# Kernel tuning notes

Measured on AMD Instinct MI355X. Metric: run time of the kernel, lower is better.

Reference implementation:

```python
import jax, jax.numpy as jnp
import numpy as np

QMAX = 127.0

def fake_quant(x):
    # per-tensor symmetric int8 fake quantize-dequantize (QAT)
    s = jnp.maximum(jnp.max(jnp.abs(x)) / QMAX, 1e-8)
    q = jnp.clip(jnp.round(x / s), -QMAX, QMAX) * s
    return x + jax.lax.stop_gradient(q - x)  # STE

def qlinear(x, w, b):
    # x already fake-quantized by caller (input_quantizer); weights fake-quantized here
    return jnp.einsum('btc,oc->bto', x, fake_quant(w)) + b

def layer_norm(x, g, b, eps=1e-5):
    m = jnp.mean(x, axis=-1, keepdims=True)
    v = jnp.var(x, axis=-1, keepdims=True)
    return (x - m) * jax.lax.rsqrt(v + eps) * g + b

def setup_inputs() -> dict:
    key = jax.random.key(0)
    ks = jax.random.split(key, 8)
    B, T, C, I = 8, 512, 1024, 4096
    sd = 0.02
    return {
        'hidden_states': jax.random.normal(ks[0], (B, T, C), jnp.float32),
        'attention_mask': jnp.ones((B, T), jnp.float32),
        'ln1_g': jnp.ones((C,), jnp.float32), 'ln1_b': jnp.zeros((C,), jnp.float32),
        'ln2_g': jnp.ones((C,), jnp.float32), 'ln2_b': jnp.zeros((C,), jnp.float32),
        'w_qkv': sd * jax.random.normal(ks[1], (3 * C, C), jnp.float32),
        'b_qkv': jnp.zeros((3 * C,), jnp.float32),
        'w_out': sd * jax.random.normal(ks[2], (C, C), jnp.float32),
        'b_out': jnp.zeros((C,), jnp.float32),
        'w1': sd * jax.random.normal(ks[3], (I, C), jnp.float32),
        'b1': jnp.zeros((I,), jnp.float32),
        'w2': sd * jax.random.normal(ks[4], (C, I), jnp.float32),
        'b2': jnp.zeros((C,), jnp.float32),
    }

def reference(hidden_states, attention_mask, ln1_g, ln1_b, ln2_g, ln2_b,
              w_qkv, b_qkv, w_out, b_out, w1, b1, w2, b2):
    B, T, C = hidden_states.shape
    H = 16
    Dh = C // H
    scale = Dh ** -0.5

    # --- attention branch (pre-norm) ---
    x = layer_norm(hidden_states, ln1_g, ln1_b)
    qkv = qlinear(fake_quant(x), w_qkv, b_qkv)            # [B,T,3C]
    qkv = qkv.reshape(B, T, 3, H, Dh).transpose(2, 0, 3, 1, 4)
    q, k, v = qkv[0], qkv[1], qkv[2]                       # [B,H,T,Dh]
    scores = jnp.einsum('bhqd,bhkd->bhqk', q, k) * scale
    ext = (1.0 - attention_mask)[:, None, None, :] * -10000.0
    scores = scores + ext
    attn = jax.nn.softmax(scores, axis=-1)
    out = jnp.einsum('bhqk,bhkd->bhqd', attn, v)
    out = out.transpose(0, 2, 1, 3).reshape(B, T, C)
    attn_out = qlinear(fake_quant(out), w_out, b_out)
    h = hidden_states + attn_out

    # --- MLP branch (pre-norm) ---
    x = layer_norm(h, ln2_g, ln2_b)
    x = qlinear(fake_quant(x), w1, b1)
    x = jax.nn.gelu(x, approximate=False)
    x = qlinear(fake_quant(x), w2, b2)
    return h + x
```

## Files before the change

kernel.cpp:

```cpp
#include <hip/hip_runtime.h>

typedef __attribute__((ext_vector_type(8))) short bf16x8;
typedef __attribute__((ext_vector_type(4))) float f32x4;
typedef __attribute__((ext_vector_type(4))) int i32x4;
typedef unsigned short u16;
typedef unsigned int u32;

#define B_ 8
#define T_ 512
#define C_ 1024
#define I_ 4096
#define H_ 16
#define Dh_ 64
#define BT (B_*T_)
#define NH (B_*H_)

__device__ __forceinline__ float bf2f(u16 u) {
  return __uint_as_float(((u32)u) << 16);
}
__device__ __forceinline__ u16 f2bf(float f) {
  u32 u = __float_as_uint(f);
  u32 r = u + 0x7FFFu + ((u >> 16) & 1u);
  return (u16)(r >> 16);
}
__device__ __forceinline__ float wredMax(float v) {
#pragma unroll
  for (int o = 32; o; o >>= 1) v = fmaxf(v, __shfl_xor(v, o));
  return v;
}
__device__ __forceinline__ float wredSum(float v) {
#pragma unroll
  for (int o = 32; o; o >>= 1) v += __shfl_xor(v, o);
  return v;
}
__device__ __forceinline__ void slotAtomicMax(u32* arr, int bid, float bm) {
  u32 b = __float_as_uint(bm);
  volatile u32* p = arr + ((bid & 63) << 4);
  if (b > *p) atomicMax((u32*)p, b);
}
__device__ __forceinline__ float slotMax(const u32* __restrict__ arr) {
  float m = 0.f;
#pragma unroll
  for (int i = 0; i < 64; ++i) m = fmaxf(m, __uint_as_float(arr[i << 4]));
  return m;
}
__device__ __forceinline__ void gload16(const void* g, void* l) {
  __builtin_amdgcn_global_load_lds((const __attribute__((address_space(1))) void*)g,
                                   (__attribute__((address_space(3))) void*)l, 16, 0, 0);
}
__device__ __forceinline__ int qi(float v, float inv) {
  return (int)fminf(fmaxf(rintf(v * inv), -127.f), 127.f);
}

__global__ void k_init(u32* s) {
  int i = blockIdx.x * 256 + threadIdx.x;
  if (i < 8192) s[i] = 0u;
}

__global__ __launch_bounds__(256) void k_absmax4(
    const float* __restrict__ p0, int n0,
    const float* __restrict__ p1, int n1,
    const float* __restrict__ p2, int n2,
    const float* __restrict__ p3, int n3,
    u32* __restrict__ sc) {
  int stride = gridDim.x * blockDim.x;
  int gid = blockIdx.x * blockDim.x + threadIdx.x;
  float m0 = 0.f, m1 = 0.f, m2 = 0.f, m3 = 0.f;
  for (int i = gid; i < n0; i += stride) {
    float4 v = ((const float4*)p0)[i];
    m0 = fmaxf(m0, fmaxf(fmaxf(fabsf(v.x), fabsf(v.y)), fmaxf(fabsf(v.z), fabsf(v.w))));
  }
  for (int i = gid; i < n1; i += stride) {
    float4 v = ((const float4*)p1)[i];
    m1 = fmaxf(m1, fmaxf(fmaxf(fabsf(v.x), fabsf(v.y)), fmaxf(fabsf(v.z), fabsf(v.w))));
  }
  for (int i = gid; i < n2; i += stride) {
    float4 v = ((const float4*)p2)[i];
    m2 = fmaxf(m2, fmaxf(fmaxf(fabsf(v.x), fabsf(v.y)), fmaxf(fabsf(v.z), fabsf(v.w))));
  }
  for (int i = gid; i < n3; i += stride) {
    float4 v = ((const float4*)p3)[i];
    m3 = fmaxf(m3, fmaxf(fmaxf(fabsf(v.x), fabsf(v.y)), fmaxf(fabsf(v.z), fabsf(v.w))));
  }
  m0 = wredMax(m0); m1 = wredMax(m1); m2 = wredMax(m2); m3 = wredMax(m3);
  __shared__ float red[4][4];
  int wid = threadIdx.x >> 6, lane = threadIdx.x & 63;
  if (lane == 0) { red[wid][0] = m0; red[wid][1] = m1; red[wid][2] = m2; red[wid][3] = m3; }
  __syncthreads();
  if (threadIdx.x < 4) {
    int j = threadIdx.x;
    float bm = fmaxf(fmaxf(red[0][j], red[1][j]), fmaxf(red[2][j], red[3][j]));
    slotAtomicMax(sc + j * 1024, blockIdx.x, bm);
  }
}

__global__ __launch_bounds__(256) void k_quant4(
    const float* __restrict__ p0, signed char* __restrict__ q0, int n0,
    const float* __restrict__ p1, signed char* __restrict__ q1, int n1,
    const float* __restrict__ p2, signed char* __restrict__ q2, int n2,
    const float* __restrict__ p3, signed char* __restrict__ q3, int n3,
    const u32* __restrict__ sc) {
  int stride = gridDim.x * blockDim.x;
  int gid = blockIdx.x * blockDim.x + threadIdx.x;
#define QLOOP(p, q, n, slot)                                                        \
  {                                                                                 \
    float s = fmaxf(slotMax(sc + slot * 1024) * (1.0f / 127.0f), 1e-8f);            \
    float inv = 1.0f / s;                                                           \
    for (int i = gid; i < n; i += stride) {                                         \
      float4 v = ((const float4*)p)[i];                                             \
      u32 pk = (u32)(qi(v.x, inv) & 255) | ((u32)(qi(v.y, inv) & 255) << 8) |       \
               ((u32)(qi(v.z, inv) & 255) << 16) | ((u32)(qi(v.w, inv) & 255) << 24); \
      ((u32*)q)[i] = pk;                                                            \
    }                                                                               \
  }
  QLOOP(p0, q0, n0, 0)
  QLOOP(p1, q1, n1, 1)
  QLOOP(p2, q2, n2, 2)
  QLOOP(p3, q3, n3, 3)
#undef QLOOP
}

__global__ __launch_bounds__(256) void k_quant_b8(const u16* __restrict__ x, signed char* __restrict__ q,
                                                  int n8, const u32* __restrict__ arr) {
  float s = fmaxf(slotMax(arr) * (1.0f / 127.0f), 1e-8f);
  float inv = 1.0f / s;
  int stride = gridDim.x * blockDim.x;
  for (int i = blockIdx.x * blockDim.x + threadIdx.x; i < n8; i += stride) {
    uint4 d = ((const uint4*)x)[i];
    u16* e = (u16*)&d;
    uint2 o;
    o.x = (u32)(qi(bf2f(e[0]), inv) & 255) | ((u32)(qi(bf2f(e[1]), inv) & 255) << 8) |
          ((u32)(qi(bf2f(e[2]), inv) & 255) << 16) | ((u32)(qi(bf2f(e[3]), inv) & 255) << 24);
    o.y = (u32)(qi(bf2f(e[4]), inv) & 255) | ((u32)(qi(bf2f(e[5]), inv) & 255) << 8) |
          ((u32)(qi(bf2f(e[6]), inv) & 255) << 16) | ((u32)(qi(bf2f(e[7]), inv) & 255) << 24);
    ((uint2*)q)[i] = o;
  }
}

__global__ __launch_bounds__(256) void k_ln(const float* __restrict__ x, const float* __restrict__ g,
                                            const float* __restrict__ b, u16* __restrict__ y,
                                            u32* __restrict__ arr) {
  int row = blockIdx.x;
  int t = threadIdx.x;
  float4 v = ((const float4*)(x + (long)row * C_))[t];
  float s1 = v.x + v.y + v.z + v.w;
  float s2 = v.x * v.x + v.y * v.y + v.z * v.z + v.w * v.w;
  s1 = wredSum(s1);
  s2 = wredSum(s2);
  __shared__ float red[8];
  int wid = t >> 6, lane = t & 63;
  if (lane == 0) { red[wid] = s1; red[4 + wid] = s2; }
  __syncthreads();
  s1 = red[0] + red[1] + red[2] + red[3];
  s2 = red[4] + red[5] + red[6] + red[7];
  float mean = s1 * (1.0f / C_);
  float var = s2 * (1.0f / C_) - mean * mean;
  float inv = rsqrtf(var + 1e-5f);
  float4 gv = ((const float4*)g)[t];
  float4 bv = ((const float4*)b)[t];
  float4 o;
  o.x = (v.x - mean) * inv * gv.x + bv.x;
  o.y = (v.y - mean) * inv * gv.y + bv.y;
  o.z = (v.z - mean) * inv * gv.z + bv.z;
  o.w = (v.w - mean) * inv * gv.w + bv.w;
  ushort4 ob;
  ob.x = f2bf(o.x); ob.y = f2bf(o.y); ob.z = f2bf(o.z); ob.w = f2bf(o.w);
  ((ushort4*)(y + (long)row * C_))[t] = ob;
  float m = fmaxf(fmaxf(fabsf(o.x), fabsf(o.y)), fmaxf(fabsf(o.z), fabsf(o.w)));
  m = wredMax(m);
  __syncthreads();
  if (lane == 0) red[wid] = m;
  __syncthreads();
  if (t == 0) {
    float bm = fmaxf(fmaxf(red[0], red[1]), fmaxf(red[2], red[3]));
    slotAtomicMax(arr, row, bm);
  }
}

__global__ __launch_bounds__(256, 1) void k_attn(
    const u16* __restrict__ qkv, const float* __restrict__ mask,
    u16* __restrict__ O, u32* __restrict__ amax) {
  __shared__ u16 Ke[512 * 64];
  __shared__ u16 Vt[64 * 512];
  __shared__ u16 Pl[4 * 64 * 40];
  __shared__ float extl[512];
  __shared__ float redm[4];
  const int tid = threadIdx.x;
  const int w = tid >> 6, l = tid & 63;
  const int head = blockIdx.x;
  const int chunk = blockIdx.y;
  const int b = head >> 4, h = head & 15;
  const long rowbase = (long)(b * 512) * (3 * C_);

  {
    const u16* Kg = qkv + rowbase + C_ + h * 64;
    int lr8 = l >> 3;
    int ls = (l & 7) ^ lr8;
    const long koff = (long)lr8 * (3 * C_) + ls * 8;
#pragma unroll
    for (int i = 0; i < 16; ++i) {
      int r0 = w * 128 + i * 8;
      gload16(Kg + (long)r0 * (3 * C_) + koff, &Ke[r0 * 64]);
    }
  }
  {
    const u16* Vg = qkv + rowbase + 2 * C_ + h * 64;
    int kvl = tid & 31;
    int d0 = (tid >> 5) * 8;
#pragma unroll 4
    for (int i = 0; i < 16; ++i) {
      int kv = i * 32 + kvl;
      uint4 t4 = *(const uint4*)(Vg + (long)kv * (3 * C_) + d0);
      u16* tv = (u16*)&t4;
      int slot = kv >> 3, within = kv & 7;
#pragma unroll
      for (int j = 0; j < 8; ++j) {
        int d = d0 + j;
        Vt[d * 512 + ((slot ^ (d & 7)) << 3) + within] = tv[j];
      }
    }
  }
  {
    const float* mb = mask + b * 512;
    extl[tid] = (1.0f - mb[tid]) * -10000.0f;
    extl[tid + 256] = (1.0f - mb[tid + 256]) * -10000.0f;
  }
  const int qbase = chunk * 256 + w * 64;
  bf16x8 qf[4][2];
  {
    const u16* Qg = qkv + rowbase + h * 64;
#pragma unroll
    for (int qt = 0; qt < 4; ++qt)
#pragma unroll
      for (int dc = 0; dc < 2; ++dc)
        qf[qt][dc] = *(const bf16x8*)(Qg + (long)(qbase + qt * 16 + (l & 15)) * (3 * C_) + dc * 32 + (l >> 4) * 8);
  }
  __syncthreads();

  f32x4 oacc[4][4];
  float mrun[4], lrun[4];
#pragma unroll
  for (int qt = 0; qt < 4; ++qt) { mrun[qt] = -3.0e38f; lrun[qt] = 0.f; }
#pragma unroll
  for (int dt = 0; dt < 4; ++dt)
#pragma unroll
    for (int qt = 0; qt < 4; ++qt) oacc[dt][qt] = (f32x4){0.f, 0.f, 0.f, 0.f};

  u16* Pw = &Pl[w * 64 * 40];

  for (int ks = 0; ks < 16; ++ks) {
    bf16x8 kf[2][2];
#pragma unroll
    for (int kvt = 0; kvt < 2; ++kvt) {
      int kv = ks * 32 + kvt * 16 + (l & 15);
#pragma unroll
      for (int dc = 0; dc < 2; ++dc) {
        int phys = (dc * 4 + (l >> 4)) ^ (kv & 7);
        kf[kvt][dc] = *(const bf16x8*)&Ke[kv * 64 + phys * 8];
      }
    }
    f32x4 sacc[2][4];
#pragma unroll
    for (int kvt = 0; kvt < 2; ++kvt)
#pragma unroll
      for (int qt = 0; qt < 4; ++qt) {
        f32x4 a = (f32x4){0.f, 0.f, 0.f, 0.f};
        a = __builtin_amdgcn_mfma_f32_16x16x32_bf16(kf[kvt][0], qf[qt][0], a, 0, 0, 0);
        a = __builtin_amdgcn_mfma_f32_16x16x32_bf16(kf[kvt][1], qf[qt][1], a, 0, 0, 0);
        sacc[kvt][qt] = a;
      }
#pragma unroll
    for (int kvt = 0; kvt < 2; ++kvt) {
      f32x4 ev = *(const f32x4*)&extl[ks * 32 + kvt * 16 + (l >> 4) * 4];
#pragma unroll
      for (int qt = 0; qt < 4; ++qt)
#pragma unroll
        for (int r = 0; r < 4; ++r)
          sacc[kvt][qt][r] = fmaf(sacc[kvt][qt][r], 0.125f, ev[r]);
    }
#pragma unroll
    for (int qt = 0; qt < 4; ++qt) {
      float pm = sacc[0][qt][0];
#pragma unroll
      for (int r = 1; r < 4; ++r) pm = fmaxf(pm, sacc[0][qt][r]);
#pragma unroll
      for (int r = 0; r < 4; ++r) pm = fmaxf(pm, sacc[1][qt][r]);
      pm = fmaxf(pm, __shfl_xor(pm, 16));
      pm = fmaxf(pm, __shfl_xor(pm, 32));
      float mnew = fmaxf(mrun[qt], pm);
      float f = __expf(mrun[qt] - mnew);
      mrun[qt] = mnew;
      float lsum = 0.f;
#pragma unroll
      for (int kvt = 0; kvt < 2; ++kvt)
#pragma unroll
        for (int r = 0; r < 4; ++r) {
          float p = __expf(sacc[kvt][qt][r] - mnew);
          sacc[kvt][qt][r] = p;
          lsum += p;
        }
      lsum += __shfl_xor(lsum, 16);
      lsum += __shfl_xor(lsum, 32);
      lrun[qt] = lrun[qt] * f + lsum;
#pragma unroll
      for (int dt = 0; dt < 4; ++dt)
#pragma unroll
        for (int r = 0; r < 4; ++r) oacc[dt][qt][r] *= f;
#pragma unroll
      for (int kvt = 0; kvt < 2; ++kvt) {
        u32 p01 = (u32)f2bf(sacc[kvt][qt][0]) | ((u32)f2bf(sacc[kvt][qt][1]) << 16);
        u32 p23 = (u32)f2bf(sacc[kvt][qt][2]) | ((u32)f2bf(sacc[kvt][qt][3]) << 16);
        u16* pr = Pw + (qt * 16 + (l & 15)) * 40 + kvt * 16 + (l >> 4) * 4;
        *(u32*)pr = p01;
        *(u32*)(pr + 2) = p23;
      }
    }
    bf16x8 vf[4], pf[4];
#pragma unroll
    for (int dt = 0; dt < 4; ++dt) {
      int d = dt * 16 + (l & 15);
      int phys = (ks * 4 + (l >> 4)) ^ (d & 7);
      vf[dt] = *(const bf16x8*)&Vt[d * 512 + phys * 8];
    }
#pragma unroll
    for (int qt = 0; qt < 4; ++qt)
      pf[qt] = *(const bf16x8*)(Pw + (qt * 16 + (l & 15)) * 40 + (l >> 4) * 8);
#pragma unroll
    for (int dt = 0; dt < 4; ++dt)
#pragma unroll
      for (int qt = 0; qt < 4; ++qt)
        oacc[dt][qt] = __builtin_amdgcn_mfma_f32_16x16x32_bf16(vf[dt], pf[qt], oacc[dt][qt], 0, 0, 0);
  }

  float lmax = 0.f;
  u16* Ob = O + (long)(b * 512 + qbase) * C_ + h * 64;
#pragma unroll
  for (int qt = 0; qt < 4; ++qt) {
    float inv = 1.0f / lrun[qt];
    long qoff = (long)(qt * 16 + (l & 15)) * C_;
#pragma unroll
    for (int dt = 0; dt < 4; ++dt) {
      int d = dt * 16 + (l >> 4) * 4;
      float v0 = oacc[dt][qt][0] * inv;
      float v1 = oacc[dt][qt][1] * inv;
      float v2 = oacc[dt][qt][2] * inv;
      float v3 = oacc[dt][qt][3] * inv;
      lmax = fmaxf(fmaxf(lmax, fmaxf(fabsf(v0), fabsf(v1))), fmaxf(fabsf(v2), fabsf(v3)));
      u32 a01 = (u32)f2bf(v0) | ((u32)f2bf(v1) << 16);
      u32 a23 = (u32)f2bf(v2) | ((u32)f2bf(v3) << 16);
      *(u32*)(Ob + qoff + d) = a01;
      *(u32*)(Ob + qoff + d + 2) = a23;
    }
  }
  lmax = wredMax(lmax);
  if (l == 0) redm[w] = lmax;
  __syncthreads();
  if (tid == 0)
    slotAtomicMax(amax, blockIdx.x * 2 + blockIdx.y,
                  fmaxf(fmaxf(redm[0], redm[1]), fmaxf(redm[2], redm[3])));
}

template <int BM, int BN, int EPI, bool SWZ>
__global__ __launch_bounds__(256) void k_gemmq(
    const signed char* __restrict__ A, int lda,
    const signed char* __restrict__ Bm, int ldb,
    const float* __restrict__ bias,
    void* __restrict__ Cp, int ldc,
    int M, int N, int K,
    const float* __restrict__ resid,
    u32* __restrict__ amaxOut,
    const u32* __restrict__ amaxA, const u32* __restrict__ amaxB) {
  constexpr int BK = 128;
  constexpr int MF = (BM / 2) / 16;
  constexpr int NF = (BN / 2) / 16;
  __shared__ __align__(16) signed char As[2][BM * BK];
  __shared__ __align__(16) signed char Bs[2][BN * BK];
  const int tid = threadIdx.x;
  const int wid = tid >> 6, lane = tid & 63;
  const int wr = wid >> 1, wc = wid & 1;

  float sa = fmaxf(slotMax(amaxA) * (1.0f / 127.0f), 1e-8f);
  float sb = fmaxf(slotMax(amaxB) * (1.0f / 127.0f), 1e-8f);
  const float sAB = sa * sb;

  int bx = blockIdx.x, by = blockIdx.y;
  if (SWZ) {
    int gx = gridDim.x;
    int nwg = gx * gridDim.y;
    int bid = by * gx + bx;
    int cpx = nwg >> 3;
    int swz = (bid & 7) * cpx + (bid >> 3);
    bx = swz % gx;
    by = swz / gx;
  }

  const signed char* Ab = A + (long)by * BM * lda;
  const signed char* Bb = Bm + (long)bx * BN * ldb;

  i32x4 acc[MF][NF];
#pragma unroll
  for (int m = 0; m < MF; m++)
#pragma unroll
    for (int n = 0; n < NF; n++) acc[m][n] = (i32x4){0, 0, 0, 0};

  const int lr = lane & 15;
  const int l8 = lane >> 3;
  const int s8 = (lane & 7) ^ l8;
  const long aoff = (long)l8 * lda + s8 * 16;
  const long boff = (long)l8 * ldb + s8 * 16;

  auto stageAB = [&](int buf, int k0) {
#pragma unroll
    for (int i = 0; i < BM / 32; ++i) {
      int R0 = wid * (BM / 4) + i * 8;
      gload16(Ab + (long)R0 * lda + k0 + aoff, &As[buf][R0 * BK]);
    }
#pragma unroll
    for (int i = 0; i < BN / 32; ++i) {
      int R0 = wid * (BN / 4) + i * 8;
      gload16(Bb + (long)R0 * ldb + k0 + boff, &Bs[buf][R0 * BK]);
    }
  };

  auto waitCounted = [&]() {
    if constexpr ((BM / 32 + BN / 32) == 8) {
      asm volatile("s_waitcnt vmcnt(8)" ::: "memory");
    } else {
      asm volatile("s_waitcnt vmcnt(6)" ::: "memory");
    }
  };

  auto computeK = [&](int buf) {
#pragma unroll
    for (int kk = 0; kk < 2; ++kk) {
      const int sl = (kk << 2) + (lane >> 4);
      const int sf = (sl ^ (lr & 7)) << 4;
      i32x4 af[MF], bfr[NF];
#pragma unroll
      for (int m = 0; m < MF; m++)
        af[m] = *(const i32x4*)&As[buf][(wr * (BM / 2) + m * 16 + lr) * BK + sf];
#pragma unroll
      for (int n = 0; n < NF; n++)
        bfr[n] = *(const i32x4*)&Bs[buf][(wc * (BN / 2) + n * 16 + lr) * BK + sf];
      __builtin_amdgcn_s_setprio(1);
#pragma unroll
      for (int m = 0; m < MF; m++)
#pragma unroll
        for (int n = 0; n < NF; n++)
          acc[m][n] = __builtin_amdgcn_mfma_i32_16x16x64_i8(af[m], bfr[n], acc[m][n], 0, 0, 0);
      __builtin_amdgcn_s_setprio(0);
    }
  };

  const int nt = K / BK;
  stageAB(0, 0);
  int cur = 0;
  for (int t = 0; t < nt; ++t) {
    if (t + 1 < nt) {
      stageAB(cur ^ 1, (t + 1) * BK);
      waitCounted();
    } else {
      asm volatile("s_waitcnt vmcnt(0)" ::: "memory");
    }
    __builtin_amdgcn_s_barrier();
    computeK(cur);
    if (t + 1 < nt)
      __builtin_amdgcn_s_barrier();
    cur ^= 1;
  }

  const int rowBase = by * BM + wr * (BM / 2);
  const int colBase = bx * BN + wc * (BN / 2);
  float lmax = 0.f;
#pragma unroll
  for (int m = 0; m < MF; m++) {
    int row0 = rowBase + m * 16 + (lane >> 4) * 4;
#pragma unroll
    for (int n = 0; n < NF; n++) {
      int col = colBase + n * 16 + lr;
      float bs = bias[col];
#pragma unroll
      for (int j = 0; j < 4; j++) {
        int row = row0 + j;
        long idx = (long)row * ldc + col;
        float v = (float)acc[m][n][j] * sAB;
        if (EPI == 0) {
          ((u16*)Cp)[idx] = f2bf(v + bs);
        } else if (EPI == 1) {
          ((float*)Cp)[idx] = v + bs + resid[idx];
        } else if (EPI == 2) {
          v += bs;
          float x2 = v * v;
          float e = __expf(v * fmaf(-0.0713548755f, x2, -1.5957691216f));
          v = v * __builtin_amdgcn_rcpf(1.0f + e);
          lmax = fmaxf(fmaxf(lmax, v), 0.0f - v);
          ((u16*)Cp)[idx] = f2bf(v);
        } else if (EPI == 3) {
          ((float*)Cp)[idx] = v + bs + resid[idx];
        }
      }
    }
  }
  if (EPI == 2) {
    __shared__ float redm[4];
    float wm = wredMax(lmax);
    if (lane == 0) redm[wid] = wm;
    __syncthreads();
    if (tid == 0) {
      float bm = fmaxf(fmaxf(redm[0], redm[1]), fmaxf(redm[2], redm[3]));
      slotAtomicMax(amaxOut, blockIdx.y * gridDim.x + blockIdx.x, bm);
    }
  }
}

extern "C" void kernel_launch(void* const* d_in, const int* in_sizes, int n_in,
                              void* d_out, int out_size, void* d_ws, size_t ws_size,
                              hipStream_t stream) {
  const float* hidden = (const float*)d_in[0];
  const float* mask = (const float*)d_in[1];
  const float* ln1g = (const float*)d_in[2];
  const float* ln1b = (const float*)d_in[3];
  const float* ln2g = (const float*)d_in[4];
  const float* ln2b = (const float*)d_in[5];
  const float* w_qkv = (const float*)d_in[6];
  const float* b_qkv = (const float*)d_in[7];
  const float* w_out = (const float*)d_in[8];
  const float* b_out = (const float*)d_in[9];
  const float* w1 = (const float*)d_in[10];
  const float* b1 = (const float*)d_in[11];
  const float* w2 = (const float*)d_in[12];
  const float* b2 = (const float*)d_in[13];

  char* ws = (char*)d_ws;
  u32* sc = (u32*)ws;
  const long MB = 1024 * 1024;
  signed char* wq_qkv = (signed char*)(ws + 1 * MB);
  signed char* wq_out = (signed char*)(ws + 4 * MB);
  signed char* wq_w1  = (signed char*)(ws + 6 * MB);
  signed char* wq_w2  = (signed char*)(ws + 10 * MB);
  signed char* xq     = (signed char*)(ws + 14 * MB);
  u16* x1             = (u16*)(ws + 18 * MB);
  signed char* Oq     = (signed char*)(ws + 26 * MB);
  u16* O              = (u16*)(ws + 30 * MB);
  u16* qkv            = (u16*)(ws + 38 * MB);
  float* hbuf         = (float*)(ws + 62 * MB);
  u16* y1             = (u16*)(ws + 78 * MB);
  signed char* y1q    = (signed char*)(ws + 110 * MB);

  k_init<<<32, 256, 0, stream>>>(sc);

  k_absmax4<<<512, 256, 0, stream>>>(
      w_qkv, 3 * C_ * C_ / 4, w_out, C_ * C_ / 4, w1, I_ * C_ / 4, w2, C_ * I_ / 4, sc);
  k_quant4<<<512, 256, 0, stream>>>(
      w_qkv, wq_qkv, 3 * C_ * C_ / 4, w_out, wq_out, C_ * C_ / 4,
      w1, wq_w1, I_ * C_ / 4, w2, wq_w2, C_ * I_ / 4, sc);

  k_ln<<<BT, 256, 0, stream>>>(hidden, ln1g, ln1b, x1, sc + 4 * 1024);
  k_quant_b8<<<512, 256, 0, stream>>>(x1, xq, BT * C_ / 8, sc + 4 * 1024);

  k_gemmq<128, 128, 0, true><<<dim3(24, 32), 256, 0, stream>>>(
      xq, C_, wq_qkv, C_, b_qkv, qkv, 3 * C_,
      BT, 3 * C_, C_, nullptr, nullptr, sc + 4 * 1024, sc + 0 * 1024);

  k_attn<<<dim3(NH, 2), 256, 0, stream>>>(qkv, mask, O, sc + 5 * 1024);
  k_quant_b8<<<512, 256, 0, stream>>>(O, Oq, BT * C_ / 8, sc + 5 * 1024);

  k_gemmq<64, 128, 1, true><<<dim3(8, 64), 256, 0, stream>>>(
      Oq, C_, wq_out, C_, b_out, hbuf, C_,
      BT, C_, C_, hidden, nullptr, sc + 5 * 1024, sc + 1 * 1024);

  k_ln<<<BT, 256, 0, stream>>>(hbuf, ln2g, ln2b, x1, sc + 6 * 1024);
  k_quant_b8<<<512, 256, 0, stream>>>(x1, xq, BT * C_ / 8, sc + 6 * 1024);

  k_gemmq<128, 128, 2, true><<<dim3(32, 32), 256, 0, stream>>>(
      xq, C_, wq_w1, C_, b1, y1, I_,
      BT, I_, C_, nullptr, sc + 7 * 1024, sc + 6 * 1024, sc + 2 * 1024);
  k_quant_b8<<<512, 256, 0, stream>>>(y1, y1q, BT * I_ / 8, sc + 7 * 1024);

  k_gemmq<64, 128, 3, true><<<dim3(8, 64), 256, 0, stream>>>(
      y1q, I_, wq_w2, I_, b2, d_out, C_,
      BT, C_, I_, hbuf, nullptr, sc + 7 * 1024, sc + 3 * 1024);
}
```

Measured before the change: 251.2 us.

## Add 256x256-tile 8-wave int8 GEMM with phased double-buffering for MLP up-projection

Replaces the generic 128x128 int8 GEMM used for the W1+GELU stage with a dedicated kernel that uses 256x256 output tiles, 512 threads (8 waves), 128-deep K tiles with XOR-swizzled LDS, and direct global-to-LDS loads. Loads for the next K tile are split across four MFMA phases, with barriers and s_setprio placed to overlap memory with compute. A block-id swizzle groups tiles for L2 reuse. The larger tiles cut global traffic per FLOP but use 128KB of LDS at one block per CU, and the grid shrinks to 256 blocks, which leaves little slack for occupancy and tail balance.

After: 249.4 us. About the same (-0.7%).

```diff
diff --git a/kernel.cpp b/kernel.cpp
--- a/kernel.cpp
+++ b/kernel.cpp
@@ -50,6 +50,11 @@
 }
 __device__ __forceinline__ int qi(float v, float inv) {
   return (int)fminf(fmaxf(rintf(v * inv), -127.f), 127.f);
+}
+__device__ __forceinline__ float gelu1(float v) {
+  float x2 = v * v;
+  float e = __expf(v * fmaf(-0.0713548755f, x2, -1.5957691216f));
+  return v * __builtin_amdgcn_rcpf(1.0f + e);
 }
 
 __global__ void k_init(u32* s) {
@@ -489,10 +494,7 @@
         } else if (EPI == 1) {
           ((float*)Cp)[idx] = v + bs + resid[idx];
         } else if (EPI == 2) {
-          v += bs;
-          float x2 = v * v;
-          float e = __expf(v * fmaf(-0.0713548755f, x2, -1.5957691216f));
-          v = v * __builtin_amdgcn_rcpf(1.0f + e);
+          v = gelu1(v + bs);
           lmax = fmaxf(fmaxf(lmax, v), 0.0f - v);
           ((u16*)Cp)[idx] = f2bf(v);
         } else if (EPI == 3) {
@@ -508,6 +510,139 @@
     __syncthreads();
     if (tid == 0) {
       float bm = fmaxf(fmaxf(redm[0], redm[1]), fmaxf(redm[2], redm[3]));
+      slotAtomicMax(amaxOut, blockIdx.y * gridDim.x + blockIdx.x, bm);
+    }
+  }
+}
+
+__global__ __launch_bounds__(512, 1) void k_gemmq8(
+    const signed char* __restrict__ A, int lda,
+    const signed char* __restrict__ Bm, int ldb,
+    const float* __restrict__ bias,
+    u16* __restrict__ Cp, int ldc,
+    int K,
+    u32* __restrict__ amaxOut,
+    const u32* __restrict__ amaxA, const u32* __restrict__ amaxB) {
+  __shared__ __align__(16) signed char As[2][256 * 128];
+  __shared__ __align__(16) signed char Bs[2][256 * 128];
+  const int tid = threadIdx.x;
+  const int wid = tid >> 6, lane = tid & 63;
+  const int wr = wid >> 2, wc = wid & 3;
+  const int lr = lane & 15;
+
+  float sa = fmaxf(slotMax(amaxA) * (1.0f / 127.0f), 1e-8f);
+  float sb = fmaxf(slotMax(amaxB) * (1.0f / 127.0f), 1e-8f);
+  const float sAB = sa * sb;
+
+  int bx = blockIdx.x, by = blockIdx.y;
+  {
+    int bid = by * 16 + bx;
+    int swz = (bid & 7) * 32 + (bid >> 3);
+    bx = swz & 15;
+    by = swz >> 4;
+  }
+  const signed char* Ab = A + (long)by * 256 * lda;
+  const signed char* Bb = Bm + (long)bx * 256 * ldb;
+
+  i32x4 acc[8][4];
+#pragma unroll
+  for (int m = 0; m < 8; m++)
+#pragma unroll
+    for (int n = 0; n < 4; n++) acc[m][n] = (i32x4){0, 0, 0, 0};
+
+  const int l8 = lane >> 3;
+  const int s8 = (lane & 7) ^ l8;
+  const long aoff = (long)l8 * lda + s8 * 16;
+  const long boff = (long)l8 * ldb + s8 * 16;
+
+  auto stageHalf = [&](int buf, int kt, int h) {
+    int k0 = kt * 128;
+    if (h < 2) {
+      int R0 = h * 128 + wid * 16;
+      gload16(Ab + (long)R0 * lda + k0 + aoff, &As[buf][R0 * 128]);
+      gload16(Ab + (long)(R0 + 8) * lda + k0 + aoff, &As[buf][(R0 + 8) * 128]);
+    } else {
+      int R0 = (h - 2) * 128 + wid * 16;
+      gload16(Bb + (long)R0 * ldb + k0 + boff, &Bs[buf][R0 * 128]);
+      gload16(Bb + (long)(R0 + 8) * ldb + k0 + boff, &Bs[buf][(R0 + 8) * 128]);
+    }
+  };
+
+  const int nt = K / 128;
+#define PHASE(BUF, Q, DOSTAGE, SBUF, SKT)                                          \
+  {                                                                                \
+    constexpr int mh = (Q) & 1, ks = (Q) >> 1;                                     \
+    const int slotl = ks * 4 + (lane >> 4);                                        \
+    i32x4 af[4], bfr[4];                                                           \
+    _Pragma("unroll") for (int i = 0; i < 4; ++i) {                                \
+      int row = wr * 128 + (mh * 4 + i) * 16 + lr;                                 \
+      af[i] = *(const i32x4*)&As[BUF][row * 128 + ((slotl ^ (row & 7)) << 4)];     \
+    }                                                                              \
+    _Pragma("unroll") for (int n = 0; n < 4; ++n) {                                \
+      int row = wc * 64 + n * 16 + lr;                                             \
+      bfr[n] = *(const i32x4*)&Bs[BUF][row * 128 + ((slotl ^ (row & 7)) << 4)];    \
+    }                                                                              \
+    if (DOSTAGE) stageHalf(SBUF, SKT, Q);                                          \
+    __builtin_amdgcn_s_barrier();                                                  \
+    __builtin_amdgcn_s_setprio(1);                                                 \
+    _Pragma("unroll") for (int i = 0; i < 4; ++i)                                  \
+      _Pragma("unroll") for (int n = 0; n < 4; ++n)                                \
+        acc[mh * 4 + i][n] =                                                       \
+            __builtin_amdgcn_mfma_i32_16x16x64_i8(af[i], bfr[n], acc[mh * 4 + i][n], 0, 0, 0); \
+    __builtin_amdgcn_s_setprio(0);                                                 \
+    __builtin_amdgcn_s_barrier();                                                  \
+  }
+
+#pragma unroll
+  for (int h = 0; h < 4; ++h) stageHalf(0, 0, h);
+
+  for (int it = 0; it < nt / 2; ++it) {
+    const int kt0 = 2 * it;
+    const bool st1 = true;
+    const bool st2 = (kt0 + 2) < nt;
+    asm volatile("s_waitcnt vmcnt(0)" ::: "memory");
+    __builtin_amdgcn_s_barrier();
+    PHASE(0, 0, st1, 1, kt0 + 1)
+    PHASE(0, 1, st1, 1, kt0 + 1)
+    PHASE(0, 2, st1, 1, kt0 + 1)
+    PHASE(0, 3, st1, 1, kt0 + 1)
+    asm volatile("s_waitcnt vmcnt(0)" ::: "memory");
+    __builtin_amdgcn_s_barrier();
+    PHASE(1, 0, st2, 0, kt0 + 2)
+    PHASE(1, 1, st2, 0, kt0 + 2)
+    PHASE(1, 2, st2, 0, kt0 + 2)
+    PHASE(1, 3, st2, 0, kt0 + 2)
+  }
+#undef PHASE
+
+  const int rowBase = by * 256 + wr * 128;
+  const int colBase = bx * 256 + wc * 64;
+  float lmax = 0.f;
+#pragma unroll
+  for (int m = 0; m < 8; m++) {
+    int row0 = rowBase + m * 16 + (lane >> 4) * 4;
+#pragma unroll
+    for (int n = 0; n < 4; n++) {
+      int col = colBase + n * 16 + lr;
+      float bs = bias[col];
+#pragma unroll
+      for (int j = 0; j < 4; j++) {
+        long idx = (long)(row0 + j) * ldc + col;
+        float v = gelu1((float)acc[m][n][j] * sAB + bs);
+        lmax = fmaxf(fmaxf(lmax, v), 0.0f - v);
+        Cp[idx] = f2bf(v);
+      }
+    }
+  }
+  {
+    __shared__ float redm[8];
+    float wm = wredMax(lmax);
+    if (lane == 0) redm[wid] = wm;
+    __syncthreads();
+    if (tid == 0) {
+      float bm = redm[0];
+#pragma unroll
+      for (int i = 1; i < 8; ++i) bm = fmaxf(bm, redm[i]);
       slotAtomicMax(amaxOut, blockIdx.y * gridDim.x + blockIdx.x, bm);
     }
   }
@@ -572,9 +707,9 @@
   k_ln<<<BT, 256, 0, stream>>>(hbuf, ln2g, ln2b, x1, sc + 6 * 1024);
   k_quant_b8<<<512, 256, 0, stream>>>(x1, xq, BT * C_ / 8, sc + 6 * 1024);
 
-  k_gemmq<128, 128, 2, true><<<dim3(32, 32), 256, 0, stream>>>(
-      xq, C_, wq_w1, C_, b1, y1, I_,
-      BT, I_, C_, nullptr, sc + 7 * 1024, sc + 6 * 1024, sc + 2 * 1024);
+  k_gemmq8<<<dim3(16, 16), 512, 0, stream>>>(
+      xq, C_, wq_w1, C_, b1, y1, I_, C_,
+      sc + 7 * 1024, sc + 6 * 1024, sc + 2 * 1024);
   k_quant_b8<<<512, 256, 0, stream>>>(y1, y1q, BT * I_ / 8, sc + 7 * 1024);
 
   k_gemmq<64, 128, 3, true><<<dim3(8, 64), 256, 0, stream>>>(
```
